# Kernel tuning notes

Hardware: AMD Instinct MI355X
Metric: run time of the kernel (lower is better)

Reference implementation:

```python
import jax, jax.numpy as jnp
import numpy as np

N = 50000
E = 800000
F_IN = 128
HEADS = 4
OUT_PER_HEAD = 32  # out_features 128 / 4 heads
NEG_SLOPE = 0.2


def setup_inputs() -> dict:
    key = jax.random.key(0)
    k1, k2, k3, k4, k5 = jax.random.split(key, 5)
    x = jax.random.normal(k1, (N, F_IN), dtype=jnp.float32)
    edge_index = jax.random.randint(k2, (2, E), 0, N, dtype=jnp.int64)
    # xavier-uniform style init
    limW = float(np.sqrt(6.0 / (F_IN + OUT_PER_HEAD)))
    W = jax.random.uniform(k3, (HEADS, F_IN, OUT_PER_HEAD), jnp.float32, -limW, limW)
    lima = float(np.sqrt(6.0 / (OUT_PER_HEAD + 1)))
    a_l = jax.random.uniform(k4, (HEADS, OUT_PER_HEAD), jnp.float32, -lima, lima)
    a_r = jax.random.uniform(k5, (HEADS, OUT_PER_HEAD), jnp.float32, -lima, lima)
    return {"x": x, "edge_index": edge_index, "W": W, "a_l": a_l, "a_r": a_r}


def _leaky_relu(v, slope):
    return jnp.where(v >= 0, v, slope * v)


def reference(x, edge_index, W, a_l, a_r):
    src, dst = edge_index[0], edge_index[1]
    n = x.shape[0]
    # Wh: [heads, N, out_per_head]
    Wh = jnp.einsum('nf,kfh->knh', x, W)
    e_l = jnp.einsum('knh,kh->kn', Wh, a_l)  # [heads, N]
    e_r = jnp.einsum('knh,kh->kn', Wh, a_r)
    # per-edge attention logits [heads, E]
    e = _leaky_relu(e_l[:, src] + e_r[:, dst], NEG_SLOPE)
    # segment softmax over incoming edges of each dst node
    seg_max = jax.vmap(lambda ee: jax.ops.segment_max(ee, dst, num_segments=n))(e)
    seg_max = jnp.maximum(seg_max, -1e9)  # torch init value for empty nodes
    exp_e = jnp.exp(e - seg_max[:, dst])
    denom = jax.vmap(lambda ee: jax.ops.segment_sum(ee, dst, num_segments=n))(exp_e)
    alpha = exp_e / (denom[:, dst] + 1e-16)  # [heads, E]
    # weighted aggregation: [heads, E, out_per_head] scattered into [heads, N, out_per_head]
    weighted = alpha[..., None] * Wh[:, src, :]
    out = jax.vmap(lambda w: jax.ops.segment_sum(w, dst, num_segments=n))(weighted)
    # concat heads -> [N, heads*out_per_head]
    return out.transpose(1, 0, 2).reshape(n, -1)
```

## Files before the change

### kernel.cpp

```cpp
#include <hip/hip_runtime.h>

#define NN 50000
#define NE 800000
#define FIN 128
#define NH 4
#define OPH 32
#define FOUT 128
#define NSLOPE 0.2f
#define NGB ((NN + 63) / 64)
#define BCOLS 144
#define LDA 136
#define BSH 5
#define BUKSZ 32
#define NBUK ((NN + BUKSZ - 1) >> BSH)
#define CHUNK 4096
#define NPB1 ((NE + CHUNK - 1) / CHUNK)
#define RSPLIT 4
#define RSPAN ((NBUK + RSPLIT - 1) / RSPLIT)
#define NPARTB (NPB1 * RSPLIT)
#define SLOTP 16
#define SLOTQ 15
#define SLOTS 64
#define GRID1 (2 * NPARTB)

typedef __attribute__((ext_vector_type(8))) short short8v;
typedef __attribute__((ext_vector_type(4))) float f32x4;

static __device__ __forceinline__ unsigned short f2bf(float f) {
  unsigned int u = __float_as_uint(f);
  u += 0x7fffu + ((u >> 16) & 1u);
  return (unsigned short)(u >> 16);
}

__global__ __launch_bounds__(128) void k_prep(
    const float* __restrict__ W, const float* __restrict__ a_l,
    const float* __restrict__ a_r, unsigned short* __restrict__ Btf) {
  const int c = blockIdx.x;
  const int f = threadIdx.x;
  unsigned short v = 0;
  if (c < 128) {
    const int h = c >> 5, o = c & 31;
    v = f2bf(W[h * (FIN * OPH) + f * OPH + o]);
  } else if (c < 136) {
    const int j = c - 128;
    const int h = j & 3;
    const float* __restrict__ av = (j < 4) ? a_l : a_r;
    float s = 0.f;
    for (int o = 0; o < 32; ++o)
      s += W[h * (FIN * OPH) + f * OPH + o] * av[h * OPH + o];
    v = f2bf(s);
  }
  const int ct = c >> 4, lr = c & 15;
  const int s = f >> 5, rem = f & 31, lk = rem >> 3, j = rem & 7;
  const int l = lr + 16 * lk;
  Btf[(((size_t)ct * 4 + s) * 64 + l) * 8 + j] = v;
}

__global__ __launch_bounds__(256) void k_gemm_part(
    const float* __restrict__ x, const unsigned short* __restrict__ Btf,
    const int* __restrict__ src, const int* __restrict__ dst,
    unsigned int* __restrict__ ebuf,
    unsigned short* __restrict__ WhU, float* __restrict__ e_l4,
    float* __restrict__ e_r4) {
  __shared__ union U {
    unsigned short As[64 * LDA];
    int cntl[RSPAN + 1];
  } sh;
  const int t = threadIdx.x;
  const int bid = blockIdx.x;

  if (bid & 1) {
    const int pidx = bid >> 1;
    const int part = pidx >> 2;
    const int r = pidx & 3;
    const int lob = r * RSPAN;
    const int hib = min(lob + RSPAN, NBUK);
    const int base = part * CHUNK;
    for (int b = t; b < RSPAN; b += 256) sh.cntl[b] = 0;
    __syncthreads();
    unsigned int* __restrict__ myreg = ebuf + (size_t)part * NBUK * SLOTP;
#pragma unroll
    for (int k = 0; k < CHUNK / 256; ++k) {
      const int i = base + k * 256 + t;
      if (i < NE) {
        const int d = dst[i];
        const int b = d >> BSH;
        if (b >= lob && b < hib) {
          const int lp = atomicAdd(&sh.cntl[b - lob], 1);
          if (lp < SLOTQ)
            myreg[b * SLOTP + 1 + lp] =
                ((unsigned int)(d & (BUKSZ - 1)) << 16) | (unsigned int)src[i];
        }
      }
    }
    __syncthreads();
    for (int b = lob + t; b < hib; b += 256)
      myreg[b * SLOTP] = (unsigned int)min(sh.cntl[b - lob], SLOTQ);
    return;
  }

  const int g = bid >> 1;
  if (g >= NGB) return;
  const int m0 = g * 64;

#pragma unroll
  for (int i = 0; i < 8; ++i) {
    const int fidx = t + i * 256;
    const int node = fidx >> 5;
    const int fg = fidx & 31;
    const int n = m0 + node;
    float4 v = make_float4(0.f, 0.f, 0.f, 0.f);
    if (n < NN) v = *(const float4*)(x + (size_t)n * FIN + fg * 4);
    ushort4 pk;
    pk.x = f2bf(v.x); pk.y = f2bf(v.y); pk.z = f2bf(v.z); pk.w = f2bf(v.w);
    *(ushort4*)&sh.As[node * LDA + fg * 4] = pk;
  }
  __syncthreads();

  const int w = t >> 6;
  const int l = t & 63;
  const int lr = l & 15;
  const int lk = l >> 4;

  short8v a_frag[4];
#pragma unroll
  for (int kk = 0; kk < 4; ++kk)
    a_frag[kk] = *(const short8v*)&sh.As[(w * 16 + lr) * LDA + kk * 32 + lk * 8];

  f32x4 acc[9];
#pragma unroll
  for (int ct = 0; ct < 9; ++ct) acc[ct] = (f32x4){0.f, 0.f, 0.f, 0.f};

#pragma unroll
  for (int ct = 0; ct < 9; ++ct) {
    const unsigned short* __restrict__ Bp = Btf + ((size_t)ct * 4) * 512 + l * 8;
    short8v b0 = *(const short8v*)(Bp);
    short8v b1 = *(const short8v*)(Bp + 512);
    short8v b2 = *(const short8v*)(Bp + 1024);
    short8v b3 = *(const short8v*)(Bp + 1536);
    acc[ct] = __builtin_amdgcn_mfma_f32_16x16x32_bf16(a_frag[0], b0, acc[ct], 0, 0, 0);
    acc[ct] = __builtin_amdgcn_mfma_f32_16x16x32_bf16(a_frag[1], b1, acc[ct], 0, 0, 0);
    acc[ct] = __builtin_amdgcn_mfma_f32_16x16x32_bf16(a_frag[2], b2, acc[ct], 0, 0, 0);
    acc[ct] = __builtin_amdgcn_mfma_f32_16x16x32_bf16(a_frag[3], b3, acc[ct], 0, 0, 0);
  }

#pragma unroll
  for (int ct = 0; ct < 9; ++ct) {
#pragma unroll
    for (int reg = 0; reg < 4; ++reg) {
      const int n = m0 + w * 16 + lk * 4 + reg;
      if (n >= NN) continue;
      const float v = acc[ct][reg];
      if (ct < 8) {
        WhU[(size_t)n * FOUT + ct * 16 + lr] = f2bf(v);
      } else if (lr < 4) {
        e_l4[n * NH + lr] = v;
      } else if (lr < 8) {
        e_r4[n * NH + (lr - 4)] = v;
      }
    }
  }
}

__global__ __launch_bounds__(256) void k_lists_agg(
    const unsigned int* __restrict__ ebuf,
    const float* __restrict__ e_l4, const float* __restrict__ e_r4,
    const unsigned int* __restrict__ Whh, float* __restrict__ out) {
  __shared__ int lists[BUKSZ][SLOTS];
  __shared__ int cur[BUKSZ];
  __shared__ float exs[4][64][4];

  const int b = blockIdx.x;
  const int t = threadIdx.x;
  const int w = t >> 6;
  const int lane = t & 63;

  if (t < BUKSZ) cur[t] = 0;
  __syncthreads();

  const int ci = lane >> 4;
  const int word = lane & 15;
#pragma unroll
  for (int it = 0; it < (NPB1 + 15) / 16; ++it) {
    const int j = it * 16 + w * 4 + ci;
    unsigned int v = 0;
    if (j < NPB1)
      v = ebuf[((size_t)j * NBUK + b) * SLOTP + word];
    const unsigned int cnt = __shfl(v, ci * 16);
    if (j < NPB1 && word >= 1 && word <= (int)cnt) {
      const int idx = (int)(v >> 16);
      const int lp = atomicAdd(&cur[idx], 1);
      if (lp < SLOTS) lists[idx][lp] = (int)(v & 0xFFFFu);
    }
  }
  __syncthreads();

  const int h = lane >> 4;
#pragma unroll
  for (int nl = 0; nl < 8; ++nl) {
    const int idx = w * 8 + nl;
    const int n = (b << BSH) + idx;
    if (n >= NN) continue;
    const int deg = min(cur[idx], SLOTS);
    const float4 ern = *(const float4*)&e_r4[n * NH];

    float e0 = 0.f, e1 = 0.f, e2 = 0.f, e3 = 0.f;
    if (lane < deg) {
      const int s = lists[idx][lane];
      const float4 el = *(const float4*)&e_l4[s * NH];
      float l0 = el.x + ern.x; l0 = (l0 >= 0.f) ? l0 : NSLOPE * l0;
      float l1 = el.y + ern.y; l1 = (l1 >= 0.f) ? l1 : NSLOPE * l1;
      float l2 = el.z + ern.z; l2 = (l2 >= 0.f) ? l2 : NSLOPE * l2;
      float l3 = el.w + ern.w; l3 = (l3 >= 0.f) ? l3 : NSLOPE * l3;
      e0 = __expf(l0); e1 = __expf(l1);
      e2 = __expf(l2); e3 = __expf(l3);
    }
    *(float4*)exs[w][lane] = make_float4(e0, e1, e2, e3);
    float D0 = e0, D1 = e1, D2 = e2, D3 = e3;
#pragma unroll
    for (int mm = 32; mm >= 1; mm >>= 1) {
      D0 += __shfl_xor(D0, mm);
      D1 += __shfl_xor(D1, mm);
      D2 += __shfl_xor(D2, mm);
      D3 += __shfl_xor(D3, mm);
    }

    float acc0 = 0.f, acc1 = 0.f;
    int jl = 0;
    for (; jl + 7 < deg; jl += 8) {
      int sj[8];
#pragma unroll
      for (int u = 0; u < 8; ++u) sj[u] = lists[idx][jl + u];
      unsigned int vv[8];
#pragma unroll
      for (int u = 0; u < 8; ++u) vv[u] = Whh[(size_t)sj[u] * 64 + lane];
#pragma unroll
      for (int u = 0; u < 8; ++u) {
        const float wH = exs[w][jl + u][h];
        acc0 = fmaf(wH, __uint_as_float(vv[u] << 16), acc0);
        acc1 = fmaf(wH, __uint_as_float(vv[u] & 0xffff0000u), acc1);
      }
    }
    for (; jl < deg; ++jl) {
      const int sj = lists[idx][jl];
      const float wH = exs[w][jl][h];
      const unsigned int v = Whh[(size_t)sj * 64 + lane];
      acc0 = fmaf(wH, __uint_as_float(v << 16), acc0);
      acc1 = fmaf(wH, __uint_as_float(v & 0xffff0000u), acc1);
    }

    const float dH = (h == 0) ? D0 : (h == 1) ? D1 : (h == 2) ? D2 : D3;
    const float inv = 1.f / (dH + 1e-16f);
    *(float2*)&out[(size_t)n * FOUT + 2 * lane] =
        make_float2(acc0 * inv, acc1 * inv);
  }
}

extern "C" void kernel_launch(void* const* d_in, const int* in_sizes, int n_in,
                              void* d_out, int out_size, void* d_ws, size_t ws_size,
                              hipStream_t stream) {
  const float* x   = (const float*)d_in[0];
  const int*   ei  = (const int*)d_in[1];
  const float* W   = (const float*)d_in[2];
  const float* a_l = (const float*)d_in[3];
  const float* a_r = (const float*)d_in[4];
  float* out = (float*)d_out;

  const int* src = ei;
  const int* dst = ei + NE;

  unsigned int* Whh = (unsigned int*)d_ws;
  float* e_l4     = (float*)(Whh + (size_t)NN * 64);
  float* e_r4     = e_l4 + NN * NH;
  unsigned short* Btf = (unsigned short*)(e_r4 + NN * NH);
  unsigned int* ebuf = (unsigned int*)(Btf + 9 * 4 * 64 * 8);
  (void)ws_size; (void)in_sizes; (void)n_in; (void)out_size;

  k_prep<<<BCOLS, 128, 0, stream>>>(W, a_l, a_r, Btf);

  k_gemm_part<<<GRID1, 256, 0, stream>>>(
      x, Btf, src, dst, ebuf, (unsigned short*)Whh, e_l4, e_r4);

  k_lists_agg<<<NBUK, 256, 0, stream>>>(ebuf, e_l4, e_r4, Whh, out);
}
```

Before: 82.02 us.

## Split each aggregation bucket across two blocks and fold denominator into accumulation loop

The aggregation kernel now launches two blocks per 32-node bucket, each handling 16 nodes and keeping only the edges whose local index falls in its half. This doubles the grid for better latency hiding and load balance, but each block still reads the full edge-buffer slice for the bucket, so those reads happen twice. The wave-wide shuffle reduction for the softmax denominator is replaced by a running sum of weights accumulated inside the gather loop, which removes the shuffles.

```diff
diff --git a/kernel.cpp b/kernel.cpp
--- a/kernel.cpp
+++ b/kernel.cpp
@@ -166,16 +166,17 @@
     const unsigned int* __restrict__ ebuf,
     const float* __restrict__ e_l4, const float* __restrict__ e_r4,
     const unsigned int* __restrict__ Whh, float* __restrict__ out) {
-  __shared__ int lists[BUKSZ][SLOTS];
-  __shared__ int cur[BUKSZ];
+  __shared__ int lists[16][SLOTS];
+  __shared__ int cur[16];
   __shared__ float exs[4][64][4];
 
-  const int b = blockIdx.x;
+  const int b = blockIdx.x >> 1;
+  const int r = blockIdx.x & 1;
   const int t = threadIdx.x;
   const int w = t >> 6;
   const int lane = t & 63;
 
-  if (t < BUKSZ) cur[t] = 0;
+  if (t < 16) cur[t] = 0;
   __syncthreads();
 
   const int ci = lane >> 4;
@@ -189,17 +190,19 @@
     const unsigned int cnt = __shfl(v, ci * 16);
     if (j < NPB1 && word >= 1 && word <= (int)cnt) {
       const int idx = (int)(v >> 16);
-      const int lp = atomicAdd(&cur[idx], 1);
-      if (lp < SLOTS) lists[idx][lp] = (int)(v & 0xFFFFu);
+      if ((idx >> 4) == r) {
+        const int lp = atomicAdd(&cur[idx & 15], 1);
+        if (lp < SLOTS) lists[idx & 15][lp] = (int)(v & 0xFFFFu);
+      }
     }
   }
   __syncthreads();
 
   const int h = lane >> 4;
 #pragma unroll
-  for (int nl = 0; nl < 8; ++nl) {
-    const int idx = w * 8 + nl;
-    const int n = (b << BSH) + idx;
+  for (int nl = 0; nl < 4; ++nl) {
+    const int idx = w * 4 + nl;
+    const int n = (b << BSH) + r * 16 + idx;
     if (n >= NN) continue;
     const int deg = min(cur[idx], SLOTS);
     const float4 ern = *(const float4*)&e_r4[n * NH];
@@ -216,16 +219,8 @@
       e2 = __expf(l2); e3 = __expf(l3);
     }
     *(float4*)exs[w][lane] = make_float4(e0, e1, e2, e3);
-    float D0 = e0, D1 = e1, D2 = e2, D3 = e3;
-#pragma unroll
-    for (int mm = 32; mm >= 1; mm >>= 1) {
-      D0 += __shfl_xor(D0, mm);
-      D1 += __shfl_xor(D1, mm);
-      D2 += __shfl_xor(D2, mm);
-      D3 += __shfl_xor(D3, mm);
-    }
-
-    float acc0 = 0.f, acc1 = 0.f;
+
+    float acc0 = 0.f, acc1 = 0.f, den = 0.f;
     int jl = 0;
     for (; jl + 7 < deg; jl += 8) {
       int sj[8];
@@ -237,6 +232,7 @@
 #pragma unroll
       for (int u = 0; u < 8; ++u) {
         const float wH = exs[w][jl + u][h];
+        den += wH;
         acc0 = fmaf(wH, __uint_as_float(vv[u] << 16), acc0);
         acc1 = fmaf(wH, __uint_as_float(vv[u] & 0xffff0000u), acc1);
       }
@@ -245,12 +241,12 @@
       const int sj = lists[idx][jl];
       const float wH = exs[w][jl][h];
       const unsigned int v = Whh[(size_t)sj * 64 + lane];
+      den += wH;
       acc0 = fmaf(wH, __uint_as_float(v << 16), acc0);
       acc1 = fmaf(wH, __uint_as_float(v & 0xffff0000u), acc1);
     }
 
-    const float dH = (h == 0) ? D0 : (h == 1) ? D1 : (h == 2) ? D2 : D3;
-    const float inv = 1.f / (dH + 1e-16f);
+    const float inv = 1.f / (den + 1e-16f);
     *(float2*)&out[(size_t)n * FOUT + 2 * lane] =
         make_float2(acc0 * inv, acc1 * inv);
   }
@@ -281,5 +277,5 @@
   k_gemm_part<<<GRID1, 256, 0, stream>>>(
       x, Btf, src, dst, ebuf, (unsigned short*)Whh, e_l4, e_r4);
 
-  k_lists_agg<<<NBUK, 256, 0, stream>>>(ebuf, e_l4, e_r4, Whh, out);
-}
+  k_lists_agg<<<2 * NBUK, 256, 0, stream>>>(ebuf, e_l4, e_r4, Whh, out);
+}
```

After: 85.20 us. 3.9% more time.

## Bin full edge chunks per block and fold softmax denominator into aggregation

Applied to the files above, without the earlier changes.

Partition blocks now each take a 4096-edge sub-chunk across all buckets, not one quarter of the bucket range, so each edge is read once instead of four times. Four sub-chunks share a 64-word bucket slot group in ebuf, and the GEMM and partition blocks are interleaved at a 4:1 ratio. The softmax denominator is now summed inside the aggregation loop, which removes the cross-lane shuffle reductions. In exchange, the shared counter array grows to cover all buckets, and every partition block must zero it and write counts for every bucket.

```diff
diff --git a/kernel.cpp b/kernel.cpp
--- a/kernel.cpp
+++ b/kernel.cpp
@@ -13,15 +13,12 @@
 #define BSH 5
 #define BUKSZ 32
 #define NBUK ((NN + BUKSZ - 1) >> BSH)
-#define CHUNK 4096
-#define NPB1 ((NE + CHUNK - 1) / CHUNK)
-#define RSPLIT 4
-#define RSPAN ((NBUK + RSPLIT - 1) / RSPLIT)
-#define NPARTB (NPB1 * RSPLIT)
-#define SLOTP 16
+#define SUBCH 4096
+#define NPSUB ((NE + SUBCH - 1) / SUBCH)
+#define NSC ((NPSUB + 3) / 4)
 #define SLOTQ 15
 #define SLOTS 64
-#define GRID1 (2 * NPARTB)
+#define GRID1 (5 * NPSUB)
 
 typedef __attribute__((ext_vector_type(8))) short short8v;
 typedef __attribute__((ext_vector_type(4))) float f32x4;
@@ -64,42 +61,39 @@
     float* __restrict__ e_r4) {
   __shared__ union U {
     unsigned short As[64 * LDA];
-    int cntl[RSPAN + 1];
+    int cntl[NBUK];
   } sh;
   const int t = threadIdx.x;
   const int bid = blockIdx.x;
 
-  if (bid & 1) {
-    const int pidx = bid >> 1;
-    const int part = pidx >> 2;
-    const int r = pidx & 3;
-    const int lob = r * RSPAN;
-    const int hib = min(lob + RSPAN, NBUK);
-    const int base = part * CHUNK;
-    for (int b = t; b < RSPAN; b += 256) sh.cntl[b] = 0;
+  if (bid % 5 == 4) {
+    const int pidx = bid / 5;
+    const int sc = pidx >> 2;
+    const int sub = pidx & 3;
+    const int base = pidx * SUBCH;
+    for (int b = t; b < NBUK; b += 256) sh.cntl[b] = 0;
     __syncthreads();
-    unsigned int* __restrict__ myreg = ebuf + (size_t)part * NBUK * SLOTP;
-#pragma unroll
-    for (int k = 0; k < CHUNK / 256; ++k) {
+    unsigned int* __restrict__ myreg =
+        ebuf + (size_t)sc * NBUK * 64 + sub * 16;
+#pragma unroll
+    for (int k = 0; k < SUBCH / 256; ++k) {
       const int i = base + k * 256 + t;
       if (i < NE) {
         const int d = dst[i];
         const int b = d >> BSH;
-        if (b >= lob && b < hib) {
-          const int lp = atomicAdd(&sh.cntl[b - lob], 1);
-          if (lp < SLOTQ)
-            myreg[b * SLOTP + 1 + lp] =
-                ((unsigned int)(d & (BUKSZ - 1)) << 16) | (unsigned int)src[i];
-        }
+        const int lp = atomicAdd(&sh.cntl[b], 1);
+        if (lp < SLOTQ)
+          myreg[(size_t)b * 64 + 1 + lp] =
+              ((unsigned int)(d & (BUKSZ - 1)) << 16) | (unsigned int)src[i];
       }
     }
     __syncthreads();
-    for (int b = lob + t; b < hib; b += 256)
-      myreg[b * SLOTP] = (unsigned int)min(sh.cntl[b - lob], SLOTQ);
+    for (int b = t; b < NBUK; b += 256)
+      myreg[(size_t)b * 64] = (unsigned int)min(sh.cntl[b], SLOTQ);
     return;
   }
 
-  const int g = bid >> 1;
+  const int g = bid - bid / 5;
   if (g >= NGB) return;
   const int m0 = g * 64;
 
@@ -178,16 +172,17 @@
   if (t < BUKSZ) cur[t] = 0;
   __syncthreads();
 
-  const int ci = lane >> 4;
   const int word = lane & 15;
 #pragma unroll
-  for (int it = 0; it < (NPB1 + 15) / 16; ++it) {
-    const int j = it * 16 + w * 4 + ci;
+  for (int it = 0; it < (NPSUB + 15) / 16; ++it) {
+    const int j = it * 16 + w * 4 + (lane >> 4);
     unsigned int v = 0;
-    if (j < NPB1)
-      v = ebuf[((size_t)j * NBUK + b) * SLOTP + word];
-    const unsigned int cnt = __shfl(v, ci * 16);
-    if (j < NPB1 && word >= 1 && word <= (int)cnt) {
+    if (j < NPSUB) {
+      const int sc = j >> 2, sub = j & 3;
+      v = ebuf[(size_t)sc * NBUK * 64 + (size_t)b * 64 + sub * 16 + word];
+    }
+    const unsigned int cnt = __shfl(v, lane & 48);
+    if (j < NPSUB && word >= 1 && word <= (int)cnt) {
       const int idx = (int)(v >> 16);
       const int lp = atomicAdd(&cur[idx], 1);
       if (lp < SLOTS) lists[idx][lp] = (int)(v & 0xFFFFu);
@@ -216,16 +211,8 @@
       e2 = __expf(l2); e3 = __expf(l3);
     }
     *(float4*)exs[w][lane] = make_float4(e0, e1, e2, e3);
-    float D0 = e0, D1 = e1, D2 = e2, D3 = e3;
-#pragma unroll
-    for (int mm = 32; mm >= 1; mm >>= 1) {
-      D0 += __shfl_xor(D0, mm);
-      D1 += __shfl_xor(D1, mm);
-      D2 += __shfl_xor(D2, mm);
-      D3 += __shfl_xor(D3, mm);
-    }
-
-    float acc0 = 0.f, acc1 = 0.f;
+
+    float acc0 = 0.f, acc1 = 0.f, den = 0.f;
     int jl = 0;
     for (; jl + 7 < deg; jl += 8) {
       int sj[8];
@@ -237,6 +224,7 @@
 #pragma unroll
       for (int u = 0; u < 8; ++u) {
         const float wH = exs[w][jl + u][h];
+        den += wH;
         acc0 = fmaf(wH, __uint_as_float(vv[u] << 16), acc0);
         acc1 = fmaf(wH, __uint_as_float(vv[u] & 0xffff0000u), acc1);
       }
@@ -245,12 +233,12 @@
       const int sj = lists[idx][jl];
       const float wH = exs[w][jl][h];
       const unsigned int v = Whh[(size_t)sj * 64 + lane];
+      den += wH;
       acc0 = fmaf(wH, __uint_as_float(v << 16), acc0);
       acc1 = fmaf(wH, __uint_as_float(v & 0xffff0000u), acc1);
     }
 
-    const float dH = (h == 0) ? D0 : (h == 1) ? D1 : (h == 2) ? D2 : D3;
-    const float inv = 1.f / (dH + 1e-16f);
+    const float inv = 1.f / (den + 1e-16f);
     *(float2*)&out[(size_t)n * FOUT + 2 * lane] =
         make_float2(acc0 * inv, acc1 * inv);
   }
```

Measured after the change: 70.02 us. 1.17x faster.
